# Optimization experiments

Hardware: AMD Instinct MI355X
Metric: run time of the kernel (lower is better)

Reference implementation:

```python
import jax, jax.numpy as jnp
import numpy as np

B, L, D, H = 2, 2048, 1024, 16
HD = D // H  # head_dim = 64


def setup_inputs() -> dict:
    key = jax.random.key(0)
    k1, k2, k3 = jax.random.split(key, 3)
    x = jax.random.normal(k1, (B, L, D), dtype=jnp.float32)
    # nn.Linear(d_model, 3*d_model): weight [3D, D], bias [3D]
    lim = 1.0 / np.sqrt(D)
    W_qkv = jax.random.uniform(k2, (3 * D, D), dtype=jnp.float32, minval=-lim, maxval=lim)
    b_qkv = jax.random.uniform(k3, (3 * D,), dtype=jnp.float32, minval=-lim, maxval=lim)
    return {"x": x, "W_qkv": W_qkv, "b_qkv": b_qkv}


def reference(x, W_qkv, b_qkv):
    b, l, d = x.shape
    qkv = x @ W_qkv.T + b_qkv                      # [b, l, 3d]
    q, k, v = jnp.split(qkv, 3, axis=-1)           # each [b, l, d]
    # split heads: [b, l, h, hd]
    q = q.reshape(b, l, H, HD)
    k = k.reshape(b, l, H, HD)
    v = v.reshape(b, l, H, HD)
    scale = 1.0 / np.sqrt(HD).astype(np.float32)
    # scores [b, h, l, l]
    scores = jnp.einsum('bqhd,bkhd->bhqk', q, k) * scale
    attn = jax.nn.softmax(scores, axis=-1)
    out = jnp.einsum('bhqk,bkhd->bqhd', attn, v)   # [b, l, h, hd]
    return out.reshape(b, l, d)
```

## Files before the change

### kernel.cpp

```cpp
#include <hip/hip_runtime.h>

#define BATCH 2
#define SEQ 2048
#define DMODEL 1024
#define NH 16
#define HD 64
#define M_TOT (BATCH*SEQ)
#define N_TOT (3*DMODEL)
#define K_TOT (DMODEL)

typedef __attribute__((ext_vector_type(8)))  _Float16 f16x8;
typedef __attribute__((ext_vector_type(4)))  float    f32x4;
typedef __attribute__((ext_vector_type(16))) float    f32x16;

static __device__ __forceinline__ unsigned short f2h(float f) {
  _Float16 h = (_Float16)f;
  return __builtin_bit_cast(unsigned short, h);
}

static __device__ __forceinline__ f32x16 zero16() {
  f32x16 z;
  #pragma unroll
  for (int i = 0; i < 16; ++i) z[i] = 0.f;
  return z;
}

static __device__ __forceinline__ void async16(const unsigned short* g, unsigned short* l) {
  __builtin_amdgcn_global_load_lds(
      (const __attribute__((address_space(1))) unsigned*)g,
      (__attribute__((address_space(3))) unsigned*)l, 16, 0, 0);
}

__global__ __launch_bounds__(256) void cast_f16(
    const float* __restrict__ src, unsigned short* __restrict__ dst, int n8)
{
  int i = blockIdx.x * 256 + threadIdx.x;
  if (i >= n8) return;
  float4 v0 = ((const float4*)src)[2*i];
  float4 v1 = ((const float4*)src)[2*i + 1];
  uint4 pk;
  pk.x = (unsigned)f2h(v0.x) | ((unsigned)f2h(v0.y) << 16);
  pk.y = (unsigned)f2h(v0.z) | ((unsigned)f2h(v0.w) << 16);
  pk.z = (unsigned)f2h(v1.x) | ((unsigned)f2h(v1.y) << 16);
  pk.w = (unsigned)f2h(v1.z) | ((unsigned)f2h(v1.w) << 16);
  ((uint4*)dst)[i] = pk;
}

__global__ __launch_bounds__(256) void qkv_gemm_mfma(
    const unsigned short* __restrict__ A,
    const unsigned short* __restrict__ B,
    const float* __restrict__ bias,
    unsigned short* __restrict__ C)
{
  __shared__ unsigned short As[128][32];
  __shared__ unsigned short Bs[128][32];

  const int tid  = threadIdx.x;
  const int wave = tid >> 6;
  const int lane = tid & 63;
  const int l15  = lane & 15;
  const int quad = lane >> 4;

  const int n0 = blockIdx.x * 128;
  const int m0 = blockIdx.y * 128;
  const int wm = (wave & 1) * 64;
  const int wn = (wave >> 1) * 64;

  f32x4 acc[4][4];
  #pragma unroll
  for (int i = 0; i < 4; ++i)
    #pragma unroll
    for (int j = 0; j < 4; ++j) acc[i][j] = (f32x4){0.f,0.f,0.f,0.f};

  const int srow = tid >> 2;
  const int skc  = (tid & 3) * 8;
  const unsigned short* Ag0 = A + (size_t)(m0 + srow) * K_TOT + skc;
  const unsigned short* Ag1 = A + (size_t)(m0 + 64 + srow) * K_TOT + skc;
  const unsigned short* Bg0 = B + (size_t)(n0 + srow) * K_TOT + skc;
  const unsigned short* Bg1 = B + (size_t)(n0 + 64 + srow) * K_TOT + skc;
  unsigned short* Al0 = &As[0][0] + tid * 8;
  unsigned short* Al1 = Al0 + 2048;
  unsigned short* Bl0 = &Bs[0][0] + tid * 8;
  unsigned short* Bl1 = Bl0 + 2048;

  for (int k0 = 0; k0 < K_TOT; k0 += 32) {
    __syncthreads();
    async16(Ag0 + k0, Al0);
    async16(Ag1 + k0, Al1);
    async16(Bg0 + k0, Bl0);
    async16(Bg1 + k0, Bl1);
    __syncthreads();

    f16x8 af[4], bf[4];
    #pragma unroll
    for (int i = 0; i < 4; ++i)
      af[i] = *(const f16x8*)&As[wm + i*16 + l15][quad*8];
    #pragma unroll
    for (int j = 0; j < 4; ++j)
      bf[j] = *(const f16x8*)&Bs[wn + j*16 + l15][quad*8];

    #pragma unroll
    for (int i = 0; i < 4; ++i)
      #pragma unroll
      for (int j = 0; j < 4; ++j)
        acc[i][j] = __builtin_amdgcn_mfma_f32_16x16x32_f16(af[i], bf[j], acc[i][j], 0, 0, 0);
  }

  float bv[4];
  #pragma unroll
  for (int j = 0; j < 4; ++j) bv[j] = bias[n0 + wn + j*16 + l15];

  #pragma unroll
  for (int i = 0; i < 4; ++i) {
    #pragma unroll
    for (int j = 0; j < 4; ++j) {
      #pragma unroll
      for (int r = 0; r < 4; ++r) {
        const size_t row = (size_t)(m0 + wm + i*16 + quad*4 + r);
        C[row * N_TOT + n0 + wn + j*16 + l15] = f2h(acc[i][j][r] + bv[j]);
      }
    }
  }
}

__global__ __launch_bounds__(256) void attn_mfma2(
    const unsigned short* __restrict__ qkv, float* __restrict__ out)
{
  __shared__ unsigned short Ks[64][72];
  __shared__ unsigned short Vt[64][72];
  __shared__ unsigned short Ps[4][32][72];
  __shared__ float Dn[4][32];

  const int tid  = threadIdx.x;
  const int wv   = tid >> 6;
  const int lane = tid & 63;
  const int l31  = lane & 31;
  const int h32  = lane >> 5;
  const int qsw  = l31 >> 3;

  const int qt = blockIdx.x;
  const int hh = blockIdx.y;
  const int b  = blockIdx.z;
  const int q0 = qt*128 + wv*32;

  f16x8 qf[4];
  {
    const unsigned short* qrow = qkv + (size_t)(b*SEQ + q0 + l31) * N_TOT + hh*HD;
    #pragma unroll
    for (int f = 0; f < 4; ++f)
      qf[f] = *(const f16x8*)(qrow + f*16 + h32*8);
  }

  f32x16 oacc[2];
  oacc[0] = zero16();
  oacc[1] = zero16();
  float dsum = 0.f;

  const unsigned short* kg = qkv + (size_t)b*SEQ*N_TOT + DMODEL   + hh*HD;
  const unsigned short* vg = qkv + (size_t)b*SEQ*N_TOT + 2*DMODEL + hh*HD;

  for (int kt = 0; kt < SEQ/64; ++kt) {
    const int k0 = kt * 64;
    __syncthreads();

    #pragma unroll
    for (int i = 0; i < 2; ++i) {
      int f   = tid + 256*i;
      int key = f >> 3, c = f & 7;
      const unsigned short* src = kg + (size_t)(k0 + key) * N_TOT + c*8;
      int sc = c ^ ((key >> 3) & 7);
      *(uint4*)&Ks[key][sc*8] = *(const uint4*)src;
    }
    {
      int key = tid >> 2;
      int d0  = (tid & 3) * 16;
      const unsigned short* src = vg + (size_t)(k0 + key) * N_TOT + d0;
      union { uint4 v; unsigned short s[8]; } u0, u1;
      u0.v = *(const uint4*)src;
      u1.v = *(const uint4*)(src + 8);
      const int kgrp = key >> 3, klow = key & 7;
      #pragma unroll
      for (int j = 0; j < 8; ++j) {
        int dd = d0 + j;
        Vt[dd][((kgrp ^ ((dd >> 3) & 7)) * 8) + klow] = u0.s[j];
        dd = d0 + 8 + j;
        Vt[dd][((kgrp ^ ((dd >> 3) & 7)) * 8) + klow] = u1.s[j];
      }
    }
    __syncthreads();

    f32x16 sa[2];
    sa[0] = zero16();
    sa[1] = zero16();
    #pragma unroll
    for (int f = 0; f < 4; ++f) {
      const int g = f*2 + h32;
      #pragma unroll
      for (int kb = 0; kb < 2; ++kb) {
        const int row = kb*32 + l31;
        f16x8 kf = *(const f16x8*)&Ks[row][((g ^ ((row >> 3) & 7)) * 8)];
        sa[kb] = __builtin_amdgcn_mfma_f32_32x32x16_f16(kf, qf[f], sa[kb], 0, 0, 0);
      }
    }

    #pragma unroll
    for (int kb = 0; kb < 2; ++kb) {
      #pragma unroll
      for (int g4 = 0; g4 < 4; ++g4) {
        unsigned short hsv[4];
        #pragma unroll
        for (int r = 0; r < 4; ++r) {
          float p = __expf(0.125f * sa[kb][g4*4 + r]);
          dsum += p;
          hsv[r] = f2h(p);
        }
        unsigned short* dst =
            &Ps[wv][l31][(((kb*4 + g4) ^ qsw) & 7) * 8 + h32*4];
        uint2 pk;
        pk.x = (unsigned)hsv[0] | ((unsigned)hsv[1] << 16);
        pk.y = (unsigned)hsv[2] | ((unsigned)hsv[3] << 16);
        *(uint2*)dst = pk;
      }
    }

    #pragma unroll
    for (int f = 0; f < 4; ++f) {
      const int g = f*2 + h32;
      f16x8 pf = *(const f16x8*)&Ps[wv][l31][((g ^ qsw) & 7) * 8];
      #pragma unroll
      for (int jd = 0; jd < 2; ++jd) {
        const int row = jd*32 + l31;
        f16x8 vf = *(const f16x8*)&Vt[row][((g ^ ((row >> 3) & 7)) * 8)];
        oacc[jd] = __builtin_amdgcn_mfma_f32_32x32x16_f16(pf, vf, oacc[jd], 0, 0, 0);
      }
    }
  }

  dsum += __shfl_xor(dsum, 32, 64);
  Dn[wv][l31] = 1.f / dsum;

  #pragma unroll
  for (int jd = 0; jd < 2; ++jd) {
    #pragma unroll
    for (int g4 = 0; g4 < 4; ++g4) {
      #pragma unroll
      for (int r = 0; r < 4; ++r) {
        const int qrow = g4*8 + h32*4 + r;
        const float oval = oacc[jd][g4*4 + r] * Dn[wv][qrow];
        out[(size_t)(b*SEQ + q0 + qrow) * DMODEL + hh*HD + jd*32 + l31] = oval;
      }
    }
  }
}

extern "C" void kernel_launch(void* const* d_in, const int* in_sizes, int n_in,
                              void* d_out, int out_size, void* d_ws, size_t ws_size,
                              hipStream_t stream) {
  const float* x    = (const float*)d_in[0];
  const float* W    = (const float*)d_in[1];
  const float* bias = (const float*)d_in[2];
  float* out = (float*)d_out;

  unsigned short* qkv = (unsigned short*)d_ws;
  unsigned short* xh  = qkv + (size_t)M_TOT * N_TOT;
  unsigned short* Wh  = xh  + (size_t)M_TOT * K_TOT;

  cast_f16<<<(M_TOT*K_TOT/8 + 255)/256, 256, 0, stream>>>(x, xh, M_TOT*K_TOT/8);
  cast_f16<<<(N_TOT*K_TOT/8 + 255)/256, 256, 0, stream>>>(W, Wh, N_TOT*K_TOT/8);

  dim3 g1(N_TOT/128, M_TOT/128);
  qkv_gemm_mfma<<<g1, 256, 0, stream>>>(xh, Wh, bias, qkv);

  dim3 g2(SEQ/128, NH, BATCH);
  attn_mfma2<<<g2, 256, 0, stream>>>(qkv, out);
}
```

Before: 192.1 us.

## Write V transposed from GEMM epilogue and pass P through registers via permlane swap

The QKV GEMM epilogue now writes the V section into a per-head transposed [b,h,d,seq] buffer, so the attention kernel loads V^T tiles with wide vector loads instead of scattering 16-bit stores into LDS. The attention kernel also drops the LDS round-trip for the probability matrix, rearranging the P fragments between lane halves with permlane32_swap (or a shuffle fallback) to feed the PV MFMA directly. It prefetches K/V into registers before the barrier and uses exp2f with a folded log2e scale. In exchange it needs extra workspace, drops the XOR swizzle on the K/Vt LDS tiles (possible bank conflicts), and makes the GEMM epilogue more strided for V.

```diff
diff --git a/kernel.cpp b/kernel.cpp
--- a/kernel.cpp
+++ b/kernel.cpp
@@ -30,6 +30,24 @@
       (const __attribute__((address_space(1))) unsigned*)g,
       (__attribute__((address_space(3))) unsigned*)l, 16, 0, 0);
 }
+
+#if __has_builtin(__builtin_amdgcn_permlane32_swap)
+static __device__ __forceinline__ void plswap(unsigned a, unsigned b,
+                                              unsigned& r0, unsigned& r1) {
+  typedef unsigned u32x2_t __attribute__((ext_vector_type(2)));
+  u32x2_t r = __builtin_amdgcn_permlane32_swap(a, b, false, false);
+  r0 = r[0]; r1 = r[1];
+}
+#else
+static __device__ __forceinline__ void plswap(unsigned a, unsigned b,
+                                              unsigned& r0, unsigned& r1) {
+  const int h32 = (threadIdx.x & 63) >> 5;
+  unsigned pa = (unsigned)__shfl_xor((int)a, 32, 64);
+  unsigned pb = (unsigned)__shfl_xor((int)b, 32, 64);
+  r0 = h32 ? pb : a;
+  r1 = h32 ? b  : pa;
+}
+#endif
 
 __global__ __launch_bounds__(256) void cast_f16(
     const float* __restrict__ src, unsigned short* __restrict__ dst, int n8)
@@ -50,7 +68,8 @@
     const unsigned short* __restrict__ A,
     const unsigned short* __restrict__ B,
     const float* __restrict__ bias,
-    unsigned short* __restrict__ C)
+    unsigned short* __restrict__ C,
+    unsigned short* __restrict__ VT)
 {
   __shared__ unsigned short As[128][32];
   __shared__ unsigned short Bs[128][32];
@@ -110,25 +129,47 @@
   #pragma unroll
   for (int j = 0; j < 4; ++j) bv[j] = bias[n0 + wn + j*16 + l15];
 
-  #pragma unroll
-  for (int i = 0; i < 4; ++i) {
-    #pragma unroll
-    for (int j = 0; j < 4; ++j) {
-      #pragma unroll
-      for (int r = 0; r < 4; ++r) {
-        const size_t row = (size_t)(m0 + wm + i*16 + quad*4 + r);
-        C[row * N_TOT + n0 + wn + j*16 + l15] = f2h(acc[i][j][r] + bv[j]);
-      }
-    }
-  }
-}
-
-__global__ __launch_bounds__(256) void attn_mfma2(
-    const unsigned short* __restrict__ qkv, float* __restrict__ out)
+  if (n0 < 2*DMODEL) {
+    #pragma unroll
+    for (int i = 0; i < 4; ++i) {
+      #pragma unroll
+      for (int j = 0; j < 4; ++j) {
+        #pragma unroll
+        for (int r = 0; r < 4; ++r) {
+          const size_t row = (size_t)(m0 + wm + i*16 + quad*4 + r);
+          C[row * N_TOT + n0 + wn + j*16 + l15] = f2h(acc[i][j][r] + bv[j]);
+        }
+      }
+    }
+  } else {
+    #pragma unroll
+    for (int i = 0; i < 4; ++i) {
+      const int m  = m0 + wm + i*16 + quad*4;
+      const int bb = m >> 11;
+      const int key = m & (SEQ - 1);
+      #pragma unroll
+      for (int j = 0; j < 4; ++j) {
+        const int vcol = n0 - 2*DMODEL + wn + j*16 + l15;
+        const int h = vcol >> 6;
+        const int d = vcol & 63;
+        unsigned lo = (unsigned)f2h(acc[i][j][0] + bv[j])
+                    | ((unsigned)f2h(acc[i][j][1] + bv[j]) << 16);
+        unsigned hi = (unsigned)f2h(acc[i][j][2] + bv[j])
+                    | ((unsigned)f2h(acc[i][j][3] + bv[j]) << 16);
+        unsigned long long pk = (unsigned long long)lo | ((unsigned long long)hi << 32);
+        *(unsigned long long*)&VT[(((size_t)bb*NH + h)*HD + d)*SEQ + key] = pk;
+      }
+    }
+  }
+}
+
+__global__ __launch_bounds__(256) void attn_mfma3(
+    const unsigned short* __restrict__ qkv,
+    const unsigned short* __restrict__ vT,
+    float* __restrict__ out)
 {
   __shared__ unsigned short Ks[64][72];
   __shared__ unsigned short Vt[64][72];
-  __shared__ unsigned short Ps[4][32][72];
   __shared__ float Dn[4][32];
 
   const int tid  = threadIdx.x;
@@ -136,7 +177,6 @@
   const int lane = tid & 63;
   const int l31  = lane & 31;
   const int h32  = lane >> 5;
-  const int qsw  = l31 >> 3;
 
   const int qt = blockIdx.x;
   const int hh = blockIdx.y;
@@ -156,36 +196,30 @@
   oacc[1] = zero16();
   float dsum = 0.f;
 
-  const unsigned short* kg = qkv + (size_t)b*SEQ*N_TOT + DMODEL   + hh*HD;
-  const unsigned short* vg = qkv + (size_t)b*SEQ*N_TOT + 2*DMODEL + hh*HD;
+  const unsigned short* kg = qkv + (size_t)b*SEQ*N_TOT + DMODEL + hh*HD;
+  const unsigned short* vg = vT + ((size_t)b*NH + hh) * HD * SEQ;
+
+  const int srow = tid >> 3;
+  const int sc   = (tid & 7) * 8;
+  const float SCL = 0.18033688011112042f;
 
   for (int kt = 0; kt < SEQ/64; ++kt) {
     const int k0 = kt * 64;
+
+    uint4 kreg[2], vreg[2];
+    #pragma unroll
+    for (int i = 0; i < 2; ++i) {
+      const int row = srow + 32*i;
+      kreg[i] = *(const uint4*)(kg + (size_t)(k0 + row) * N_TOT + sc);
+      vreg[i] = *(const uint4*)(vg + (size_t)row * SEQ + k0 + sc);
+    }
+
     __syncthreads();
-
     #pragma unroll
     for (int i = 0; i < 2; ++i) {
-      int f   = tid + 256*i;
-      int key = f >> 3, c = f & 7;
-      const unsigned short* src = kg + (size_t)(k0 + key) * N_TOT + c*8;
-      int sc = c ^ ((key >> 3) & 7);
-      *(uint4*)&Ks[key][sc*8] = *(const uint4*)src;
-    }
-    {
-      int key = tid >> 2;
-      int d0  = (tid & 3) * 16;
-      const unsigned short* src = vg + (size_t)(k0 + key) * N_TOT + d0;
-      union { uint4 v; unsigned short s[8]; } u0, u1;
-      u0.v = *(const uint4*)src;
-      u1.v = *(const uint4*)(src + 8);
-      const int kgrp = key >> 3, klow = key & 7;
-      #pragma unroll
-      for (int j = 0; j < 8; ++j) {
-        int dd = d0 + j;
-        Vt[dd][((kgrp ^ ((dd >> 3) & 7)) * 8) + klow] = u0.s[j];
-        dd = d0 + 8 + j;
-        Vt[dd][((kgrp ^ ((dd >> 3) & 7)) * 8) + klow] = u1.s[j];
-      }
+      const int row = srow + 32*i;
+      *(uint4*)&Ks[row][sc] = kreg[i];
+      *(uint4*)&Vt[row][sc] = vreg[i];
     }
     __syncthreads();
 
@@ -194,44 +228,40 @@
     sa[1] = zero16();
     #pragma unroll
     for (int f = 0; f < 4; ++f) {
-      const int g = f*2 + h32;
       #pragma unroll
       for (int kb = 0; kb < 2; ++kb) {
-        const int row = kb*32 + l31;
-        f16x8 kf = *(const f16x8*)&Ks[row][((g ^ ((row >> 3) & 7)) * 8)];
+        f16x8 kf = *(const f16x8*)&Ks[kb*32 + l31][f*16 + h32*8];
         sa[kb] = __builtin_amdgcn_mfma_f32_32x32x16_f16(kf, qf[f], sa[kb], 0, 0, 0);
       }
     }
 
+    unsigned Dw[2][8];
     #pragma unroll
     for (int kb = 0; kb < 2; ++kb) {
       #pragma unroll
-      for (int g4 = 0; g4 < 4; ++g4) {
-        unsigned short hsv[4];
+      for (int rr = 0; rr < 8; ++rr) {
+        float p0 = exp2f(sa[kb][2*rr]   * SCL);
+        float p1 = exp2f(sa[kb][2*rr+1] * SCL);
+        dsum += p0 + p1;
+        Dw[kb][rr] = (unsigned)f2h(p0) | ((unsigned)f2h(p1) << 16);
+      }
+    }
+
+    #pragma unroll
+    for (int kb = 0; kb < 2; ++kb) {
+      #pragma unroll
+      for (int c2 = 0; c2 < 2; ++c2) {
+        unsigned F0, F1, F2, F3;
+        plswap(Dw[kb][c2*4+0], Dw[kb][c2*4+2], F0, F2);
+        plswap(Dw[kb][c2*4+1], Dw[kb][c2*4+3], F1, F3);
+        union { unsigned u[4]; f16x8 v; } pk;
+        pk.u[0] = F0; pk.u[1] = F1; pk.u[2] = F2; pk.u[3] = F3;
+        const int kc = kb*2 + c2;
         #pragma unroll
-        for (int r = 0; r < 4; ++r) {
-          float p = __expf(0.125f * sa[kb][g4*4 + r]);
-          dsum += p;
-          hsv[r] = f2h(p);
+        for (int jd = 0; jd < 2; ++jd) {
+          f16x8 vf = *(const f16x8*)&Vt[jd*32 + l31][kc*16 + h32*8];
+          oacc[jd] = __builtin_amdgcn_mfma_f32_32x32x16_f16(pk.v, vf, oacc[jd], 0, 0, 0);
         }
-        unsigned short* dst =
-            &Ps[wv][l31][(((kb*4 + g4) ^ qsw) & 7) * 8 + h32*4];
-        uint2 pk;
-        pk.x = (unsigned)hsv[0] | ((unsigned)hsv[1] << 16);
-        pk.y = (unsigned)hsv[2] | ((unsigned)hsv[3] << 16);
-        *(uint2*)dst = pk;
-      }
-    }
-
-    #pragma unroll
-    for (int f = 0; f < 4; ++f) {
-      const int g = f*2 + h32;
-      f16x8 pf = *(const f16x8*)&Ps[wv][l31][((g ^ qsw) & 7) * 8];
-      #pragma unroll
-      for (int jd = 0; jd < 2; ++jd) {
-        const int row = jd*32 + l31;
-        f16x8 vf = *(const f16x8*)&Vt[row][((g ^ ((row >> 3) & 7)) * 8)];
-        oacc[jd] = __builtin_amdgcn_mfma_f32_32x32x16_f16(pf, vf, oacc[jd], 0, 0, 0);
       }
     }
   }
@@ -264,13 +294,14 @@
   unsigned short* qkv = (unsigned short*)d_ws;
   unsigned short* xh  = qkv + (size_t)M_TOT * N_TOT;
   unsigned short* Wh  = xh  + (size_t)M_TOT * K_TOT;
+  unsigned short* vTp = Wh  + (size_t)N_TOT * K_TOT;
 
   cast_f16<<<(M_TOT*K_TOT/8 + 255)/256, 256, 0, stream>>>(x, xh, M_TOT*K_TOT/8);
   cast_f16<<<(N_TOT*K_TOT/8 + 255)/256, 256, 0, stream>>>(W, Wh, N_TOT*K_TOT/8);
 
   dim3 g1(N_TOT/128, M_TOT/128);
-  qkv_gemm_mfma<<<g1, 256, 0, stream>>>(xh, Wh, bias, qkv);
+  qkv_gemm_mfma<<<g1, 256, 0, stream>>>(xh, Wh, bias, qkv, vTp);
 
   dim3 g2(SEQ/128, NH, BATCH);
-  attn_mfma2<<<g2, 256, 0, stream>>>(qkv, out);
-}
+  attn_mfma3<<<g2, 256, 0, stream>>>(qkv, vTp, out);
+}
```

Measured after the change: 242.8 us. 26.4% more time.
